# Kernel tuning notes

Hardware: AMD Instinct MI355X
Metric: run time of the kernel (lower is better)

## Reference

```python
import jax, jax.numpy as jnp
import numpy as np

C = 1.0          # Poincare ball curvature
H = 8            # num_heads
EPS = 1e-15
DELTA = 1e-7
SC = np.sqrt(C)  # sqrt curvature


def _norm(x):
    return jnp.sqrt(jnp.clip(jnp.sum(x * x, -1, keepdims=True), 1e-15))


def mobius_add(x, y):
    xy = jnp.sum(x * y, -1, keepdims=True)
    x2 = jnp.sum(x * x, -1, keepdims=True)
    y2 = jnp.sum(y * y, -1, keepdims=True)
    num = (1 + 2 * C * xy + C * y2) * x + (1 - C * x2) * y
    den = 1 + 2 * C * xy + C * C * x2 * y2
    return num / (den + EPS)


def mobius_matvec(W, x):
    xn = _norm(x)
    mx = x @ W.T
    mxn = _norm(mx)
    arg = jnp.clip(SC * xn, None, 1 - 1e-5)
    return jnp.tanh(mxn / xn * jnp.arctanh(arg)) * mx / (mxn * SC)


def logmap0(x):
    xn = _norm(x)
    return jnp.arctanh(jnp.clip(SC * xn, None, 1 - 1e-5)) * x / (SC * xn)


def expmap0(u):
    un = _norm(u)
    return jnp.tanh(SC * un) * u / (SC * un)


def hyp_linear(W, b, x):
    return mobius_add(mobius_matvec(W, x), b)


def setup_inputs() -> dict:
    key = jax.random.key(0)
    ks = jax.random.split(key, 5)
    B, S, E = 2, 512, 256
    x = jax.random.normal(ks[0], (B, S, E), jnp.float32) * 0.02  # inside unit ball
    scale = float(np.sqrt(6.0 / (E + E)))  # xavier uniform bound
    Wq = jax.random.uniform(ks[1], (E, E), jnp.float32, -scale, scale)
    Wk = jax.random.uniform(ks[2], (E, E), jnp.float32, -scale, scale)
    Wv = jax.random.uniform(ks[3], (E, E), jnp.float32, -scale, scale)
    Wo = jax.random.uniform(ks[4], (E, E), jnp.float32, -scale, scale)
    z = jnp.zeros((E,), jnp.float32)
    head_scaling = jnp.ones((H, 1, 1), jnp.float32)
    return {"x": x, "Wq": Wq, "bq": z, "Wk": Wk, "bk": z, "Wv": Wv, "bv": z,
            "Wo": Wo, "bo": z, "head_scaling": head_scaling}


def reference(x, Wq, bq, Wk, bk, Wv, bv, Wo, bo, head_scaling):
    B, S, E = x.shape
    D = E // H
    q = hyp_linear(Wq, bq, x).reshape(B, S, H, D).transpose(0, 2, 1, 3)  # (B,H,S,D)
    k = hyp_linear(Wk, bk, x).reshape(B, S, H, D).transpose(0, 2, 1, 3)
    v = hyp_linear(Wv, bv, x).reshape(B, S, H, D).transpose(0, 2, 1, 3)
    max_norm = (1 - 1e-5) / SC
    q = jnp.minimum(q, max_norm)  # elementwise clamp_max, faithful to source
    k = jnp.minimum(k, max_norm)
    qn = C * jnp.sum(q * q, -1)[..., :, None]   # (B,H,Sq,1)
    kn = C * jnp.sum(k * k, -1)[..., None, :]   # (B,H,1,Sk)
    # pairwise mobius_add(-k, q): (B,H,Sq,Sk,D)
    diff = mobius_add(-k[:, :, None, :, :], q[:, :, :, None, :])
    dn = C * jnp.sum(diff * diff, -1)           # (B,H,Sq,Sk)
    denom = (1 - qn) * (1 - kn) + EPS
    a = jnp.maximum(1 + 2 * dn / denom, 1 + DELTA)
    dist = jnp.log(a + jnp.sqrt(a * a - 1))     # acosh
    scores = -dist / (head_scaling * np.sqrt(D))
    w = jax.nn.softmax(scores, -1)
    out = expmap0(jnp.einsum('bhqk,bhkd->bhqd', w, logmap0(v)))
    out = out.transpose(0, 2, 1, 3).reshape(B, S, E)
    return hyp_linear(Wo, bo, out)
```

## Files before the change

### kernel.cpp

```cpp
#include <hip/hip_runtime.h>
#include <math.h>

#define Ec 256
#define Sc 512
#define Bc 2
#define Hc 8
#define Dc 32
#define MAXNORM (1.0f - 1e-5f)
#define NEc (Bc * Sc * Ec)
#define KSQ 2
#define KSO 4
#define NROWS (Bc * Hc * Sc)
#define KT 128
#define NT (Sc / KT)

__device__ __forceinline__ float fullWaveSum(float v) {
#pragma unroll
  for (int m = 32; m >= 1; m >>= 1) v += __shfl_xor(v, m, 64);
  return v;
}
__device__ __forceinline__ float halfWaveSum(float v) {
#pragma unroll
  for (int m = 16; m >= 1; m >>= 1) v += __shfl_xor(v, m, 64);
  return v;
}
__device__ __forceinline__ float atanh_fast(float z) {
  return 0.5f * __logf((1.0f + z) / (1.0f - z));
}
__device__ __forceinline__ float tanh_fast(float a) {
  float e = __expf(-2.0f * a);
  return (1.0f - e) / (1.0f + e);
}

__global__ __launch_bounds__(128) void gemm_xwt(
    const float* __restrict__ X,
    const float* __restrict__ W0, const float* __restrict__ W1,
    const float* __restrict__ W2,
    float* __restrict__ O0, float* __restrict__ O1, float* __restrict__ O2,
    const int nk) {
  const int tid = threadIdx.x;
  const int bx = blockIdx.x;
  const int by = blockIdx.y;
  const int kz = blockIdx.z;
  const int mat = by >> 2;
  const int cb0 = (by & 3) * 64;
  const int rb0 = bx * 32;
  const int kk0 = kz * 64 * nk;
  const float* __restrict__ W = (mat == 0) ? W0 : (mat == 1) ? W1 : W2;
  float* __restrict__ O = ((mat == 0) ? O0 : (mat == 1) ? O1 : O2) + (size_t)kz * NEc;

  __shared__ float Xs[64][36];
  __shared__ float Ws[64][68];

  const int f4 = tid & 15;
  const int sub = tid >> 4;
  const int ty = tid >> 4;
  const int tx = tid & 15;

  float acc[4][4];
#pragma unroll
  for (int i = 0; i < 4; ++i)
#pragma unroll
    for (int j = 0; j < 4; ++j) acc[i][j] = 0.f;

  for (int c = 0; c < nk; ++c) {
    const int kk = kk0 + c * 64;
    __syncthreads();
#pragma unroll
    for (int i = 0; i < 4; ++i) {
      int row = sub + i * 8;
      float4 v = *(const float4*)&X[(size_t)(rb0 + row) * Ec + kk + f4 * 4];
      Xs[f4 * 4 + 0][row] = v.x;
      Xs[f4 * 4 + 1][row] = v.y;
      Xs[f4 * 4 + 2][row] = v.z;
      Xs[f4 * 4 + 3][row] = v.w;
    }
#pragma unroll
    for (int i = 0; i < 8; ++i) {
      int col = sub + i * 8;
      float4 v = *(const float4*)&W[(size_t)(cb0 + col) * Ec + kk + f4 * 4];
      Ws[f4 * 4 + 0][col] = v.x;
      Ws[f4 * 4 + 1][col] = v.y;
      Ws[f4 * 4 + 2][col] = v.z;
      Ws[f4 * 4 + 3][col] = v.w;
    }
    __syncthreads();
#pragma unroll 8
    for (int k = 0; k < 64; ++k) {
      float4 a = *(const float4*)&Xs[k][ty * 4];
      float4 b = *(const float4*)&Ws[k][tx * 4];
      float av[4] = {a.x, a.y, a.z, a.w};
      float bv[4] = {b.x, b.y, b.z, b.w};
#pragma unroll
      for (int i = 0; i < 4; ++i)
#pragma unroll
        for (int j = 0; j < 4; ++j) acc[i][j] = fmaf(av[i], bv[j], acc[i][j]);
    }
  }
#pragma unroll
  for (int i = 0; i < 4; ++i) {
    float4 o = make_float4(acc[i][0], acc[i][1], acc[i][2], acc[i][3]);
    *(float4*)&O[(size_t)(rb0 + ty * 4 + i) * Ec + cb0 + tx * 4] = o;
  }
}

__global__ __launch_bounds__(256) void qkv_stats(
    const float* __restrict__ x,
    const float* __restrict__ mxq, const float* __restrict__ mxk,
    const float* __restrict__ mxv,
    const float* __restrict__ bq, const float* __restrict__ bk,
    const float* __restrict__ bv,
    float* __restrict__ qo, float* __restrict__ ko, float* __restrict__ lvo,
    float* __restrict__ qno, float* __restrict__ kno) {
  const int t = threadIdx.x;
  const int row = blockIdx.x;
  const int b = row >> 9;
  const int s = row & (Sc - 1);
  const size_t idx = (size_t)row * Ec + t;
  const float xv = x[idx];
  float mq = 0.f, mk = 0.f, mv = 0.f;
#pragma unroll
  for (int p = 0; p < KSQ; ++p) {
    mq += mxq[idx + (size_t)p * NEc];
    mk += mxk[idx + (size_t)p * NEc];
    mv += mxv[idx + (size_t)p * NEc];
  }
  const float bb[3] = {bq[t], bk[t], bv[t]};
  const float mvals[3] = {mq, mk, mv};

  float vals[10] = {xv * xv,
                    mq * mq, mq * bb[0], bb[0] * bb[0],
                    mk * mk, mk * bb[1], bb[1] * bb[1],
                    mv * mv, mv * bb[2], bb[2] * bb[2]};
  __shared__ float red[10][4];
  __shared__ float fin[10];
#pragma unroll
  for (int i = 0; i < 10; ++i) {
    float v = fullWaveSum(vals[i]);
    if ((t & 63) == 0) red[i][t >> 6] = v;
  }
  __syncthreads();
  if (t < 10) fin[t] = red[t][0] + red[t][1] + red[t][2] + red[t][3];
  __syncthreads();

  const float x2 = fin[0];
  const float xn = sqrtf(fmaxf(x2, 1e-15f));
  const float at = atanh_fast(fminf(xn, MAXNORM));
  const int h = t >> 5;

#pragma unroll
  for (int m = 0; m < 3; ++m) {
    float mx2 = fin[1 + 3 * m];
    float mxb = fin[2 + 3 * m];
    float b2 = fin[3 + 3 * m];
    float mxn = sqrtf(fmaxf(mx2, 1e-15f));
    float scl = tanh_fast((mxn / xn) * at) / mxn;
    float mvv = scl * mvals[m];
    float X2 = scl * scl * mx2;
    float XY = scl * mxb;
    float numc = 1.0f + 2.0f * XY + b2;
    float den = 1.0f + 2.0f * XY + X2 * b2 + 1e-15f;
    float res = (numc * mvv + (1.0f - X2) * bb[m]) / den;
    if (m < 2) {
      res = fminf(res, MAXNORM);
      float s2 = halfWaveSum(res * res);
      if (m == 0) {
        qo[idx] = res;
        if ((t & 31) == 0) qno[(b * Hc + h) * Sc + s] = s2;
      } else {
        ko[idx] = res;
        if ((t & 31) == 0) kno[(b * Hc + h) * Sc + s] = s2;
      }
    } else {
      float vn2 = halfWaveSum(res * res);
      float vn = sqrtf(fmaxf(vn2, 1e-15f));
      float f = atanh_fast(fminf(vn, MAXNORM)) / vn;
      lvo[idx] = f * res;
    }
  }
}

__global__ __launch_bounds__(256, 2) void attn_fused(
    const float* __restrict__ q, const float* __restrict__ k,
    const float* __restrict__ lv, const float* __restrict__ qn,
    const float* __restrict__ kn, const float* __restrict__ hs,
    float* __restrict__ out) {
  const int tid = threadIdx.x;
  const int sq0 = blockIdx.x * 16;
  const int bh = blockIdx.y;
  const int b = bh >> 3;
  const int h = bh & 7;

  __shared__ float Qst[16][36];
  __shared__ float Kst[32][132];
  __shared__ float LVs[128][36];
  __shared__ float Pst[16][132];
  __shared__ float knS[128];
  __shared__ float accm[16][8][32];
  __shared__ float lsb[16][9];

  const int r2 = tid >> 5;
  const int c4 = tid & 31;
  const int js = tid >> 5;
  const int rg = (tid >> 3) & 3;
  const int dq = tid & 7;
  const int rr = tid >> 1;
  const int half = tid & 1;

  if (tid < 128) {
    int qr = tid >> 3, dqq = tid & 7;
    *(float4*)&Qst[qr][dqq * 4] =
        *(const float4*)&q[(size_t)(b * Sc + sq0 + qr) * Ec + h * Dc + dqq * 4];
  }
  __syncthreads();
  float4 qv0[8], qv1[8];
#pragma unroll
  for (int fd = 0; fd < 8; ++fd) {
    qv0[fd] = *(const float4*)&Qst[2 * r2 + 0][fd * 4];
    qv1[fd] = *(const float4*)&Qst[2 * r2 + 1][fd * 4];
  }
  const float q20 = qn[bh * Sc + sq0 + 2 * r2];
  const float q21 = qn[bh * Sc + sq0 + 2 * r2 + 1];
  const float omq0 = 1.0f - q20;
  const float omq1 = 1.0f - q21;
  const float sinv = -1.0f / (hs[h] * sqrtf((float)Dc));

  float4 acc[4];
#pragma unroll
  for (int i = 0; i < 4; ++i) acc[i] = make_float4(0.f, 0.f, 0.f, 0.f);
  float lsum4[4] = {0.f, 0.f, 0.f, 0.f};

  for (int t = 0; t < NT; ++t) {
    const int j0g = t * KT;
    __syncthreads();
    {
      const size_t gbase = (size_t)(b * Sc + j0g + rr) * Ec + h * Dc;
#pragma unroll
      for (int i = 0; i < 4; ++i) {
        const int dqq = half * 4 + i;
        float4 kv = *(const float4*)&k[gbase + dqq * 4];
        Kst[dqq * 4 + 0][rr] = kv.x;
        Kst[dqq * 4 + 1][rr] = kv.y;
        Kst[dqq * 4 + 2][rr] = kv.z;
        Kst[dqq * 4 + 3][rr] = kv.w;
        *(float4*)&LVs[rr][dqq * 4] = *(const float4*)&lv[gbase + dqq * 4];
      }
      if (tid < 128) knS[tid] = kn[bh * Sc + j0g + tid];
    }
    __syncthreads();

    float p0[4] = {0.f, 0.f, 0.f, 0.f};
    float p1[4] = {0.f, 0.f, 0.f, 0.f};
#pragma unroll
    for (int fd = 0; fd < 8; ++fd) {
      float4 k0 = *(const float4*)&Kst[fd * 4 + 0][c4 * 4];
      float4 k1 = *(const float4*)&Kst[fd * 4 + 1][c4 * 4];
      float4 k2 = *(const float4*)&Kst[fd * 4 + 2][c4 * 4];
      float4 k3 = *(const float4*)&Kst[fd * 4 + 3][c4 * 4];
      float4 a0 = qv0[fd];
      float4 a1 = qv1[fd];
      p0[0] = fmaf(a0.x, k0.x, p0[0]); p0[0] = fmaf(a0.y, k1.x, p0[0]);
      p0[0] = fmaf(a0.z, k2.x, p0[0]); p0[0] = fmaf(a0.w, k3.x, p0[0]);
      p0[1] = fmaf(a0.x, k0.y, p0[1]); p0[1] = fmaf(a0.y, k1.y, p0[1]);
      p0[1] = fmaf(a0.z, k2.y, p0[1]); p0[1] = fmaf(a0.w, k3.y, p0[1]);
      p0[2] = fmaf(a0.x, k0.z, p0[2]); p0[2] = fmaf(a0.y, k1.z, p0[2]);
      p0[2] = fmaf(a0.z, k2.z, p0[2]); p0[2] = fmaf(a0.w, k3.z, p0[2]);
      p0[3] = fmaf(a0.x, k0.w, p0[3]); p0[3] = fmaf(a0.y, k1.w, p0[3]);
      p0[3] = fmaf(a0.z, k2.w, p0[3]); p0[3] = fmaf(a0.w, k3.w, p0[3]);
      p1[0] = fmaf(a1.x, k0.x, p1[0]); p1[0] = fmaf(a1.y, k1.x, p1[0]);
      p1[0] = fmaf(a1.z, k2.x, p1[0]); p1[0] = fmaf(a1.w, k3.x, p1[0]);
      p1[1] = fmaf(a1.x, k0.y, p1[1]); p1[1] = fmaf(a1.y, k1.y, p1[1]);
      p1[1] = fmaf(a1.z, k2.y, p1[1]); p1[1] = fmaf(a1.w, k3.y, p1[1]);
      p1[2] = fmaf(a1.x, k0.z, p1[2]); p1[2] = fmaf(a1.y, k1.z, p1[2]);
      p1[2] = fmaf(a1.z, k2.z, p1[2]); p1[2] = fmaf(a1.w, k3.z, p1[2]);
      p1[3] = fmaf(a1.x, k0.w, p1[3]); p1[3] = fmaf(a1.y, k1.w, p1[3]);
      p1[3] = fmaf(a1.z, k2.w, p1[3]); p1[3] = fmaf(a1.w, k3.w, p1[3]);
    }

    float4 k2v = *(const float4*)&knS[c4 * 4];
    const float kk2[4] = {k2v.x, k2v.y, k2v.z, k2v.w};
    {
      float po[4];
#pragma unroll
      for (int j = 0; j < 4; ++j) {
        const float k2 = kk2[j];
        const float kq = p0[j];
        const float omk = 1.0f - k2;
        float s2x2 = fmaf(-4.0f, kq, 2.0f * k2 + 2.0f * q20);
        float dden = fmaf(k2, q20, fmaf(-2.0f, kq, 1.0f)) + 1e-15f;
        float Pd = fmaf(dden, omk * omq0, 1e-20f);
        float rp = __builtin_amdgcn_rcpf(Pd);
        float tt = fmaxf(s2x2 * rp, 1e-7f);
        float z = (1.0f + tt) + sqrtf(fmaf(tt, tt, tt + tt));
        po[j] = __builtin_amdgcn_exp2f(sinv * __builtin_amdgcn_logf(z));
      }
      *(float4*)&Pst[2 * r2 + 0][c4 * 4] = make_float4(po[0], po[1], po[2], po[3]);
    }
    {
      float po[4];
#pragma unroll
      for (int j = 0; j < 4; ++j) {
        const float k2 = kk2[j];
        const float kq = p1[j];
        const float omk = 1.0f - k2;
        float s2x2 = fmaf(-4.0f, kq, 2.0f * k2 + 2.0f * q21);
        float dden = fmaf(k2, q21, fmaf(-2.0f, kq, 1.0f)) + 1e-15f;
        float Pd = fmaf(dden, omk * omq1, 1e-20f);
        float rp = __builtin_amdgcn_rcpf(Pd);
        float tt = fmaxf(s2x2 * rp, 1e-7f);
        float z = (1.0f + tt) + sqrtf(fmaf(tt, tt, tt + tt));
        po[j] = __builtin_amdgcn_exp2f(sinv * __builtin_amdgcn_logf(z));
      }
      *(float4*)&Pst[2 * r2 + 1][c4 * 4] = make_float4(po[0], po[1], po[2], po[3]);
    }
    __syncthreads();

#pragma unroll
    for (int j4 = 0; j4 < 4; ++j4) {
      const int jl = js * 16 + j4 * 4;
      float4 p[4], l[4];
#pragma unroll
      for (int i = 0; i < 4; ++i) p[i] = *(const float4*)&Pst[rg * 4 + i][jl];
#pragma unroll
      for (int c = 0; c < 4; ++c) l[c] = *(const float4*)&LVs[jl + c][dq * 4];
#pragma unroll
      for (int i = 0; i < 4; ++i) {
        lsum4[i] += (p[i].x + p[i].y) + (p[i].z + p[i].w);
        acc[i].x = fmaf(p[i].x, l[0].x, acc[i].x);
        acc[i].y = fmaf(p[i].x, l[0].y, acc[i].y);
        acc[i].z = fmaf(p[i].x, l[0].z, acc[i].z);
        acc[i].w = fmaf(p[i].x, l[0].w, acc[i].w);
        acc[i].x = fmaf(p[i].y, l[1].x, acc[i].x);
        acc[i].y = fmaf(p[i].y, l[1].y, acc[i].y);
        acc[i].z = fmaf(p[i].y, l[1].z, acc[i].z);
        acc[i].w = fmaf(p[i].y, l[1].w, acc[i].w);
        acc[i].x = fmaf(p[i].z, l[2].x, acc[i].x);
        acc[i].y = fmaf(p[i].z, l[2].y, acc[i].y);
        acc[i].z = fmaf(p[i].z, l[2].z, acc[i].z);
        acc[i].w = fmaf(p[i].z, l[2].w, acc[i].w);
        acc[i].x = fmaf(p[i].w, l[3].x, acc[i].x);
        acc[i].y = fmaf(p[i].w, l[3].y, acc[i].y);
        acc[i].z = fmaf(p[i].w, l[3].z, acc[i].z);
        acc[i].w = fmaf(p[i].w, l[3].w, acc[i].w);
      }
    }
  }

#pragma unroll
  for (int i = 0; i < 4; ++i)
    *(float4*)&accm[rg * 4 + i][js][dq * 4] = acc[i];
  if (dq == 0) {
#pragma unroll
    for (int i = 0; i < 4; ++i) lsb[rg * 4 + i][js] = lsum4[i];
  }
  __syncthreads();

  const int r2e = tid >> 4;
  const int dd = tid & 15;
  float o0 = 0.f, o1 = 0.f, ls = 0.f;
#pragma unroll
  for (int g = 0; g < 8; ++g) {
    float2 a2 = *(const float2*)&accm[r2e][g][dd * 2];
    o0 += a2.x;
    o1 += a2.y;
    ls += lsb[r2e][g];
  }
  const float li = 1.0f / ls;
  o0 *= li;
  o1 *= li;
  float un2 = fmaf(o0, o0, o1 * o1);
#pragma unroll
  for (int m = 8; m >= 1; m >>= 1) un2 += __shfl_xor(un2, m, 16);
  float un = sqrtf(fmaxf(un2, 1e-15f));
  float f = tanh_fast(un) / un;
  float2 ov = make_float2(o0 * f, o1 * f);
  *(float2*)&out[(size_t)(b * Sc + sq0 + r2e) * Ec + h * Dc + dd * 2] = ov;
}

__global__ __launch_bounds__(256) void proj_stats(
    const float* __restrict__ xin, const float* __restrict__ mx,
    const float* __restrict__ bo, float* __restrict__ out) {
  const int t = threadIdx.x;
  const int row = blockIdx.x;
  const size_t idx = (size_t)row * Ec + t;
  const float xv = xin[idx];
  float m = 0.f;
#pragma unroll
  for (int p = 0; p < KSO; ++p) m += mx[idx + (size_t)p * NEc];
  const float bb = bo[t];
  float vals[4] = {xv * xv, m * m, m * bb, bb * bb};
  __shared__ float red[4][4];
  __shared__ float fin[4];
#pragma unroll
  for (int i = 0; i < 4; ++i) {
    float v = fullWaveSum(vals[i]);
    if ((t & 63) == 0) red[i][t >> 6] = v;
  }
  __syncthreads();
  if (t < 4) fin[t] = red[t][0] + red[t][1] + red[t][2] + red[t][3];
  __syncthreads();

  float x2 = fin[0], mx2 = fin[1], mxb = fin[2], b2 = fin[3];
  float xn = sqrtf(fmaxf(x2, 1e-15f));
  float mxn = sqrtf(fmaxf(mx2, 1e-15f));
  float scl = tanh_fast((mxn / xn) * atanh_fast(fminf(xn, MAXNORM))) / mxn;
  float mvv = scl * m;
  float X2 = scl * scl * mx2;
  float XY = scl * mxb;
  float numc = 1.0f + 2.0f * XY + b2;
  float den = 1.0f + 2.0f * XY + X2 * b2 + 1e-15f;
  out[idx] = (numc * mvv + (1.0f - X2) * bb) / den;
}

extern "C" void kernel_launch(void* const* d_in, const int* in_sizes, int n_in,
                              void* d_out, int out_size, void* d_ws, size_t ws_size,
                              hipStream_t stream) {
  (void)in_sizes; (void)n_in; (void)out_size; (void)ws_size;
  const float* x  = (const float*)d_in[0];
  const float* Wq = (const float*)d_in[1];
  const float* bq = (const float*)d_in[2];
  const float* Wk = (const float*)d_in[3];
  const float* bk = (const float*)d_in[4];
  const float* Wv = (const float*)d_in[5];
  const float* bv = (const float*)d_in[6];
  const float* Wo = (const float*)d_in[7];
  const float* bo = (const float*)d_in[8];
  const float* hs = (const float*)d_in[9];

  float* ws = (float*)d_ws;
  const int NE = NEc;
  const int NH = NROWS;
  float* mxq = ws;
  float* mxk = mxq + KSQ * NE;
  float* mxv = mxk + KSQ * NE;
  float* mxo = mxv + KSQ * NE;
  float* qb  = mxo + KSO * NE;
  float* kb  = qb + NE;
  float* lvb = kb + NE;
  float* aob = lvb + NE;
  float* qnb = aob + NE;
  float* knb = qnb + NH;

  const int M = Bc * Sc;

  gemm_xwt<<<dim3(M / 32, 12, KSQ), 128, 0, stream>>>(x, Wq, Wk, Wv,
                                                      mxq, mxk, mxv, 2);
  qkv_stats<<<M, 256, 0, stream>>>(x, mxq, mxk, mxv, bq, bk, bv,
                                   qb, kb, lvb, qnb, knb);
  attn_fused<<<dim3(32, 16), 256, 0, stream>>>(qb, kb, lvb, qnb, knb, hs, aob);
  gemm_xwt<<<dim3(M / 32, 4, KSO), 128, 0, stream>>>(aob, Wo, Wo, Wo,
                                                     mxo, mxo, mxo, 1);
  proj_stats<<<M, 256, 0, stream>>>(aob, mxo, bo, (float*)d_out);
}
```

Baseline: 124.6 us.

## Enlarge GEMM row tile to 64 with 4x8 micro-tiles and deeper split-K

The X·Wᵀ GEMM now uses 64x64 output tiles, with each thread computing a 4x8 register block instead of 4x4. This raises FMA work per shared-memory load. To keep the QKV grid size unchanged, split-K for the QKV projection goes from 2 to 4 with one 64-wide K chunk per split. The cost is more partial-sum traffic for the stats kernel to reduce, more register pressure, and half as many blocks for the output projection.

```diff
diff --git a/kernel.cpp b/kernel.cpp
--- a/kernel.cpp
+++ b/kernel.cpp
@@ -8,7 +8,7 @@
 #define Dc 32
 #define MAXNORM (1.0f - 1e-5f)
 #define NEc (Bc * Sc * Ec)
-#define KSQ 2
+#define KSQ 4
 #define KSO 4
 #define NROWS (Bc * Hc * Sc)
 #define KT 128
@@ -44,63 +44,62 @@
   const int kz = blockIdx.z;
   const int mat = by >> 2;
   const int cb0 = (by & 3) * 64;
-  const int rb0 = bx * 32;
+  const int rb0 = bx * 64;
   const int kk0 = kz * 64 * nk;
   const float* __restrict__ W = (mat == 0) ? W0 : (mat == 1) ? W1 : W2;
   float* __restrict__ O = ((mat == 0) ? O0 : (mat == 1) ? O1 : O2) + (size_t)kz * NEc;
 
-  __shared__ float Xs[64][36];
+  __shared__ float Xs[64][68];
   __shared__ float Ws[64][68];
 
   const int f4 = tid & 15;
   const int sub = tid >> 4;
-  const int ty = tid >> 4;
-  const int tx = tid & 15;
-
-  float acc[4][4];
+  const int r4 = tid >> 3;
+  const int c8 = tid & 7;
+
+  float acc[4][8];
 #pragma unroll
   for (int i = 0; i < 4; ++i)
 #pragma unroll
-    for (int j = 0; j < 4; ++j) acc[i][j] = 0.f;
+    for (int j = 0; j < 8; ++j) acc[i][j] = 0.f;
 
   for (int c = 0; c < nk; ++c) {
     const int kk = kk0 + c * 64;
     __syncthreads();
 #pragma unroll
-    for (int i = 0; i < 4; ++i) {
+    for (int i = 0; i < 8; ++i) {
       int row = sub + i * 8;
       float4 v = *(const float4*)&X[(size_t)(rb0 + row) * Ec + kk + f4 * 4];
       Xs[f4 * 4 + 0][row] = v.x;
       Xs[f4 * 4 + 1][row] = v.y;
       Xs[f4 * 4 + 2][row] = v.z;
       Xs[f4 * 4 + 3][row] = v.w;
-    }
-#pragma unroll
-    for (int i = 0; i < 8; ++i) {
-      int col = sub + i * 8;
-      float4 v = *(const float4*)&W[(size_t)(cb0 + col) * Ec + kk + f4 * 4];
-      Ws[f4 * 4 + 0][col] = v.x;
-      Ws[f4 * 4 + 1][col] = v.y;
-      Ws[f4 * 4 + 2][col] = v.z;
-      Ws[f4 * 4 + 3][col] = v.w;
+      float4 w = *(const float4*)&W[(size_t)(cb0 + row) * Ec + kk + f4 * 4];
+      Ws[f4 * 4 + 0][row] = w.x;
+      Ws[f4 * 4 + 1][row] = w.y;
+      Ws[f4 * 4 + 2][row] = w.z;
+      Ws[f4 * 4 + 3][row] = w.w;
     }
     __syncthreads();
 #pragma unroll 8
     for (int k = 0; k < 64; ++k) {
-      float4 a = *(const float4*)&Xs[k][ty * 4];
-      float4 b = *(const float4*)&Ws[k][tx * 4];
+      float4 a = *(const float4*)&Xs[k][r4 * 4];
+      float4 b0 = *(const float4*)&Ws[k][c8 * 8];
+      float4 b1 = *(const float4*)&Ws[k][c8 * 8 + 4];
       float av[4] = {a.x, a.y, a.z, a.w};
-      float bv[4] = {b.x, b.y, b.z, b.w};
+      float bv[8] = {b0.x, b0.y, b0.z, b0.w, b1.x, b1.y, b1.z, b1.w};
 #pragma unroll
       for (int i = 0; i < 4; ++i)
 #pragma unroll
-        for (int j = 0; j < 4; ++j) acc[i][j] = fmaf(av[i], bv[j], acc[i][j]);
+        for (int j = 0; j < 8; ++j) acc[i][j] = fmaf(av[i], bv[j], acc[i][j]);
     }
   }
 #pragma unroll
   for (int i = 0; i < 4; ++i) {
-    float4 o = make_float4(acc[i][0], acc[i][1], acc[i][2], acc[i][3]);
-    *(float4*)&O[(size_t)(rb0 + ty * 4 + i) * Ec + cb0 + tx * 4] = o;
+    float4 o0 = make_float4(acc[i][0], acc[i][1], acc[i][2], acc[i][3]);
+    float4 o1 = make_float4(acc[i][4], acc[i][5], acc[i][6], acc[i][7]);
+    *(float4*)&O[(size_t)(rb0 + r4 * 4 + i) * Ec + cb0 + c8 * 8] = o0;
+    *(float4*)&O[(size_t)(rb0 + r4 * 4 + i) * Ec + cb0 + c8 * 8 + 4] = o1;
   }
 }
 
@@ -443,12 +442,12 @@
 
   const int M = Bc * Sc;
 
-  gemm_xwt<<<dim3(M / 32, 12, KSQ), 128, 0, stream>>>(x, Wq, Wk, Wv,
-                                                      mxq, mxk, mxv, 2);
+  gemm_xwt<<<dim3(M / 64, 12, KSQ), 128, 0, stream>>>(x, Wq, Wk, Wv,
+                                                      mxq, mxk, mxv, 1);
   qkv_stats<<<M, 256, 0, stream>>>(x, mxq, mxk, mxv, bq, bk, bv,
                                    qb, kb, lvb, qnb, knb);
   attn_fused<<<dim3(32, 16), 256, 0, stream>>>(qb, kb, lvb, qnb, knb, hs, aob);
-  gemm_xwt<<<dim3(M / 32, 4, KSO), 128, 0, stream>>>(aob, Wo, Wo, Wo,
+  gemm_xwt<<<dim3(M / 64, 4, KSO), 128, 0, stream>>>(aob, Wo, Wo, Wo,
                                                      mxo, mxo, mxo, 1);
   proj_stats<<<M, 256, 0, stream>>>(aob, mxo, bo, (float*)d_out);
 }
```

Measured after the change: 122.9 us, median of 2. About the same (-1.4%).
